# Optimization experiments

Measured on AMD Instinct MI355X. Metric: run time of the kernel, lower is better.

Reference implementation:

```python
import jax, jax.numpy as jnp
import numpy as np

K = 5        # spline kernel_size per dim (dim=2 -> 25 kernel weights)
NPG = 75     # MNIST superpixel nodes per graph


def _spline_conv(x, src, dst, pseudo, emask, W, root, bias):
    """SplineConv, dim=2, kernel_size=5, degree=1 open splines, aggr='mean'.
    emask in {0,1} masks out coalesced-away (duplicate/self-loop) edges."""
    n = x.shape[0]
    v = jnp.clip(pseudo, 0.0, 1.0) * (K - 1)
    bot = jnp.clip(jnp.floor(v), 0, K - 2)
    frac = v - bot                                   # [E,2]
    bot = bot.astype(jnp.int32)
    xj = x[src] * emask[:, None]                     # [E,Fin] gathered source feats
    # aggregate-then-transform: acc[k,i,:] = sum over edges into i with basis k
    acc = jnp.zeros((K * K, n, x.shape[1]), x.dtype)
    for o0 in (0, 1):
        for o1 in (0, 1):
            w = (frac[:, 0] if o0 else 1.0 - frac[:, 0]) * (frac[:, 1] if o1 else 1.0 - frac[:, 1])
            kk = (bot[:, 0] + o0) + K * (bot[:, 1] + o1)
            acc = acc.at[kk, dst].add(w[:, None] * xj)
    out = jnp.einsum('knf,kfo->no', acc, W)
    deg = jax.ops.segment_sum(emask, dst, num_segments=n)
    return out / jnp.maximum(deg, 1.0)[:, None] + x @ root + bias


def _pool(x, pos, valid, batch, src, dst, emask, size, G, B):
    """voxel_grid + max_pool with static shapes: S=B*G*G clusters, masked."""
    S = B * G * G
    c = jnp.clip(jnp.floor(pos / size).astype(jnp.int32), 0, G - 1)
    cl = batch * (G * G) + c[:, 1] * G + c[:, 0]
    xm = jnp.where(valid[:, None] > 0, x, -1e30)
    px = jax.ops.segment_max(xm, cl, num_segments=S)
    cnt = jax.ops.segment_sum(valid, cl, num_segments=S)
    sval = (cnt > 0).astype(x.dtype)
    px = jnp.where(sval[:, None] > 0, px, 0.0)
    ppos = jax.ops.segment_sum(pos * valid[:, None], cl, num_segments=S) / jnp.maximum(cnt, 1.0)[:, None]
    nb = jnp.arange(S, dtype=jnp.int32) // (G * G)
    # remap edges to clusters; mask self loops and duplicates (= coalesce)
    nsrc, ndst = cl[src], cl[dst]
    m = (emask > 0) & (nsrc != ndst)
    a0 = jnp.where(m, nsrc, S)
    b0 = jnp.where(m, ndst, S)
    order = jnp.lexsort((b0, a0))
    a, b = a0[order], b0[order]
    first = jnp.concatenate([jnp.array([True]), (a[1:] != a[:-1]) | (b[1:] != b[:-1])])
    keep = jnp.zeros(src.shape[0], dtype=bool).at[order].set(first & (a < S))
    kf = keep.astype(x.dtype)
    # T.Cartesian(cat=False, norm=True): pseudo = (pos_src-pos_dst)/(2*max|.|)+0.5
    cart = ppos[nsrc] - ppos[ndst]
    amax = jnp.maximum(jnp.max(jnp.abs(cart) * kf[:, None]), 1e-12)
    pseudo = cart / (2.0 * amax) + 0.5
    return px, ppos, sval, nb, nsrc, ndst, kf, pseudo


def _forward(x, pos, src, dst, W1, r1, b1, W2, r2, b2, W3, r3, b3, fw1, fb1, fw2, fb2):
    N = x.shape[0]
    B = N // NPG
    batch = jnp.arange(N, dtype=jnp.int32) // NPG
    valid = jnp.ones((N,), x.dtype)
    emask = jnp.ones((src.shape[0],), x.dtype)
    cart = pos[src] - pos[dst]
    pseudo = cart / (2.0 * jnp.maximum(jnp.max(jnp.abs(cart)), 1e-12)) + 0.5
    x = jax.nn.elu(_spline_conv(x, src, dst, pseudo, emask, W1, r1, b1))
    x, pos, valid, batch, src, dst, emask, pseudo = _pool(x, pos, valid, batch, src, dst, emask, 5.0, 6, B)
    x = jax.nn.elu(_spline_conv(x, src, dst, pseudo, emask, W2, r2, b2))
    x, pos, valid, batch, src, dst, emask, pseudo = _pool(x, pos, valid, batch, src, dst, emask, 7.0, 5, B)
    x = jax.nn.elu(_spline_conv(x, src, dst, pseudo, emask, W3, r3, b3))
    # max_pool_x(cluster, x, batch, size=4): 2x2 voxel grid (size=14, end=27.99)
    c = jnp.clip(jnp.floor(pos / 14.0).astype(jnp.int32), 0, 1)
    cl = batch * 4 + c[:, 1] * 2 + c[:, 0]
    xm = jnp.where(valid[:, None] > 0, x, -1e30)
    px = jax.ops.segment_max(xm, cl, num_segments=B * 4)
    cnt = jax.ops.segment_sum(valid, cl, num_segments=B * 4)
    px = jnp.where((cnt > 0)[:, None], px, 0.0)
    h = jax.nn.elu(px.reshape(B, 4 * 64) @ fw1.T + fb1)
    logits = h @ fw2.T + fb2  # F.dropout is identity in eval mode
    return jax.nn.log_softmax(logits, axis=1)


def setup_inputs() -> dict:
    key = jax.random.key(0)
    ks = jax.random.split(key, 16)
    B, EPG = 1024, 1392
    N = B * NPG
    x = jax.random.normal(ks[0], (N, 1), jnp.float32)
    pos = jax.random.uniform(ks[1], (N, 2), jnp.float32) * 27.99
    s = jax.random.randint(ks[2], (B, EPG), 0, NPG)
    d = (s + 1 + jax.random.randint(ks[3], (B, EPG), 0, NPG - 1)) % NPG  # no self loops
    off = (jnp.arange(B, dtype=jnp.int32) * NPG)[:, None]
    src = (s + off).reshape(-1)
    dst = (d + off).reshape(-1)
    rn = lambda k, sh, sc: jax.random.normal(k, sh, jnp.float32) * sc
    return dict(x=x, pos=pos, src=src, dst=dst,
                W1=rn(ks[4], (25, 1, 32), 0.2), r1=rn(ks[5], (1, 32), 0.2), b1=jnp.zeros((32,), jnp.float32),
                W2=rn(ks[6], (25, 32, 64), 0.05), r2=rn(ks[7], (32, 64), 0.1), b2=jnp.zeros((64,), jnp.float32),
                W3=rn(ks[8], (25, 64, 64), 0.04), r3=rn(ks[9], (64, 64), 0.08), b3=jnp.zeros((64,), jnp.float32),
                fw1=rn(ks[10], (128, 256), 0.06), fb1=jnp.zeros((128,), jnp.float32),
                fw2=rn(ks[11], (10, 128), 0.09), fb2=jnp.zeros((10,), jnp.float32))


def reference(x, pos, src, dst, W1, r1, b1, W2, r2, b2, W3, r3, b3, fw1, fb1, fw2, fb2):
    return _forward(x, pos, src, dst, W1, r1, b1, W2, r2, b2, W3, r3, b3, fw1, fb1, fw2, fb2)
```

## Files before the change

kernel.cpp:

```cpp
#include <hip/hip_runtime.h>
#include <math.h>

#define NPG 75
#define KDIM 5

typedef _Float16 half8 __attribute__((ext_vector_type(8)));
typedef _Float16 half4 __attribute__((ext_vector_type(4)));
typedef float f32x4 __attribute__((ext_vector_type(4)));

__device__ __forceinline__ float eluf(float v){ return v > 0.f ? v : expf(v) - 1.f; }

__device__ __forceinline__ unsigned fenc(float f){
    unsigned u = __float_as_uint(f);
    return (u & 0x80000000u) ? ~u : (u | 0x80000000u);
}
__device__ __forceinline__ float fdec(unsigned u){
    return (u & 0x80000000u) ? __uint_as_float(u & 0x7FFFFFFFu) : __uint_as_float(~u);
}

__device__ __forceinline__ void fma25(float (&r)[25], const float (&wx)[5], const float (&wyx)[5]){
    #pragma unroll
    for (int b1 = 0; b1 < 5; b1++)
        #pragma unroll
        for (int b0 = 0; b0 < 5; b0++)
            asm("v_fmac_f32 %0, %1, %2" : "+v"(r[b1 * 5 + b0]) : "v"(wx[b0]), "v"(wyx[b1]));
}

__device__ __forceinline__ void spline2(float c0, float c1, float am, int* kks, float* wsp){
    float denom = 2.f * fmaxf(am, 1e-12f);
    float p0 = c0 / denom + 0.5f;
    float p1 = c1 / denom + 0.5f;
    p0 = fminf(fmaxf(p0, 0.f), 1.f) * 4.f;
    p1 = fminf(fmaxf(p1, 0.f), 1.f) * 4.f;
    float b0 = fminf(floorf(p0), 3.f);
    float b1 = fminf(floorf(p1), 3.f);
    float f0 = p0 - b0, f1 = p1 - b1;
    int i0 = (int)b0, i1 = (int)b1;
    wsp[0] = (1.f - f0) * (1.f - f1); kks[0] = i0     + KDIM *  i1;
    wsp[1] =        f0  * (1.f - f1); kks[1] = i0 + 1 + KDIM *  i1;
    wsp[2] = (1.f - f0) *        f1 ; kks[2] = i0     + KDIM * (i1 + 1);
    wsp[3] =        f0  *        f1 ; kks[3] = i0 + 1 + KDIM * (i1 + 1);
}

__global__ __launch_bounds__(256) void amax0_k(
        const float* __restrict__ pos, const int* __restrict__ src,
        const int* __restrict__ dst, int E4, unsigned* __restrict__ outbits){
    float cand = 0.f;
    for (int i = blockIdx.x * 256 + threadIdx.x; i < E4; i += gridDim.x * 256){
        int4 s4 = ((const int4*)src)[i];
        int4 d4 = ((const int4*)dst)[i];
        #pragma unroll
        for (int k = 0; k < 4; k++){
            int s = (&s4.x)[k], d = (&d4.x)[k];
            float c0 = pos[s*2]   - pos[d*2];
            float c1 = pos[s*2+1] - pos[d*2+1];
            cand = fmaxf(cand, fmaxf(fabsf(c0), fabsf(c1)));
        }
    }
    __shared__ float sm[256];
    sm[threadIdx.x] = cand; __syncthreads();
    for (int o = 128; o > 0; o >>= 1){
        if (threadIdx.x < o) sm[threadIdx.x] = fmaxf(sm[threadIdx.x], sm[threadIdx.x + o]);
        __syncthreads();
    }
    if (threadIdx.x == 0) atomicMax(outbits, __float_as_uint(sm[0]));
}

__global__ __launch_bounds__(512) void conv1pool1_k(
        const float* __restrict__ x, const float* __restrict__ pos,
        const int* __restrict__ src, const int* __restrict__ dst, int EPG,
        const unsigned* __restrict__ amaxp,
        const float* __restrict__ W1, const float* __restrict__ r1, const float* __restrict__ b1,
        float* __restrict__ px1, float* __restrict__ pp1, float* __restrict__ sv1,
        int* __restrict__ cl1){
    __shared__ __align__(16) float acc[NPG * 28];
    __shared__ float deg[NPG];
    __shared__ float xl[NPG], p0l[NPG], p1l[NPG];
    __shared__ int   cli[NPG];
    __shared__ float W1s[800], r1s[32], b1s[32];
    __shared__ unsigned px[36 * 32];
    __shared__ float cnt[36], ps[72];

    const int b = blockIdx.x, t = threadIdx.x;
    const int n0 = b * NPG, e0 = b * EPG;

    for (int i = t; i < NPG * 28; i += 512) acc[i] = 0.f;
    for (int i = t; i < 36 * 32; i += 512) px[i] = 0u;
    if (t < NPG) deg[t] = 0.f;
    if (t < 36) cnt[t] = 0.f;
    if (t < 72) ps[t] = 0.f;
    for (int i = t; i < 800; i += 512) W1s[i] = W1[i];
    if (t < 32){ r1s[t] = r1[t]; b1s[t] = b1[t]; }
    if (t < NPG){
        float p0 = pos[(n0 + t) * 2], p1 = pos[(n0 + t) * 2 + 1];
        xl[t] = x[n0 + t]; p0l[t] = p0; p1l[t] = p1;
        int c0 = min(max((int)floorf(p0 / 5.f), 0), 5);
        int c1 = min(max((int)floorf(p1 / 5.f), 0), 5);
        int c = c1 * 6 + c0;
        cli[t] = c;
        cl1[n0 + t] = b * 36 + c;
    }
    __syncthreads();

    const int o = t & 31;
    float wreg[25];
    #pragma unroll
    for (int k = 0; k < 25; k++) wreg[k] = W1s[k * 32 + o];
    const float rro = r1s[o], bbo = b1s[o];

    if (t < NPG){
        int c = cli[t];
        atomicAdd(&cnt[c], 1.f);
        atomicAdd(&ps[c*2],     p0l[t]);
        atomicAdd(&ps[c*2 + 1], p1l[t]);
    }

    const float am = __uint_as_float(*amaxp);
    for (int e = t; e < EPG; e += 512){
        int s = src[e0 + e] - n0;
        int d = dst[e0 + e] - n0;
        float c0 = p0l[s] - p0l[d];
        float c1 = p1l[s] - p1l[d];
        int kks[4]; float wsp[4];
        spline2(c0, c1, am, kks, wsp);
        float xv = xl[s];
        #pragma unroll
        for (int c = 0; c < 4; c++) atomicAdd(&acc[d*28 + kks[c]], wsp[c] * xv);
        atomicAdd(&deg[d], 1.f);
    }
    __syncthreads();

    const int ii = t >> 5;
    #pragma unroll
    for (int r = 0; r < 5; r++){
        int i = ii + r * 16;
        if (i < NPG){
            const float4* ar = (const float4*)(acc + i * 28);
            float s = 0.f;
            #pragma unroll
            for (int q = 0; q < 7; q++){
                float4 aq = ar[q];
                s += aq.x * wreg[q*4];
                if (q*4 + 1 < 25) s += aq.y * wreg[q*4 + 1];
                if (q*4 + 2 < 25) s += aq.z * wreg[q*4 + 2];
                if (q*4 + 3 < 25) s += aq.w * wreg[q*4 + 3];
            }
            float v = s / fmaxf(deg[i], 1.f) + xl[i] * rro + bbo;
            v = eluf(v);
            atomicMax(&px[cli[i]*32 + o], fenc(v));
        }
    }
    __syncthreads();

    for (int idx = t; idx < 36 * 32; idx += 512){
        int s_ = idx >> 5;
        px1[(size_t)(b*36)*32 + idx] = (cnt[s_] > 0.f) ? fdec(px[idx]) : 0.f;
    }
    if (t < 36){
        float c = cnt[t], m = fmaxf(c, 1.f);
        pp1[(b*36 + t)*2]     = ps[t*2] / m;
        pp1[(b*36 + t)*2 + 1] = ps[t*2 + 1] / m;
        sv1[b*36 + t] = (c > 0.f) ? 1.f : 0.f;
    }
}

template<int GG, int NN>
__global__ __launch_bounds__(1024) void dedup_csr_k(
        const int* src_in, const int* dst_in,
        const int* __restrict__ clmap, const unsigned char* __restrict__ kf_in,
        unsigned char* kf_out, int* es_out, int* ed_out,
        const float* __restrict__ pp, int EPG,
        int* __restrict__ easrc, float2* __restrict__ ecart,
        int* __restrict__ rowptr2, int* __restrict__ kcnt, unsigned* __restrict__ amaxbits){
    __shared__ unsigned pm[GG * GG];
    __shared__ float degs[GG];
    __shared__ int rs[GG + 1];
    __shared__ int cur[GG];
    __shared__ float red[16];
    __shared__ int   clS[NN];
    __shared__ float ppS[2 * GG];

    const int b = blockIdx.x, t = threadIdx.x;
    const int lane = t & 63, wid = t >> 6;
    const int e0 = b * EPG;
    const int cbase = b * GG;

    for (int i = t; i < GG * GG; i += 1024) pm[i] = 0xFFFFFFFFu;
    if (t < GG) degs[t] = 0.f;
    if (t < NN) clS[t] = clmap[b * NN + t] - cbase;
    if (t < 2 * GG) ppS[t] = pp[cbase * 2 + t];
    __syncthreads();

    const int niter = (EPG + 1023) / 1024;
    int la[2], lb[2]; bool lm[2];
    const int nbase = b * NN;
    for (int it = 0; it < niter; it++){
        int e = t + it * 1024;
        lm[it] = false;
        if (e < EPG){
            int a  = clS[src_in[e0 + e] - nbase];
            int bb = clS[dst_in[e0 + e] - nbase];
            la[it] = a; lb[it] = bb;
            es_out[e0 + e] = cbase + a; ed_out[e0 + e] = cbase + bb;
            bool m = (kf_in ? (kf_in[e0 + e] != 0) : true) && (a != bb);
            lm[it] = m;
            if (m) atomicMin(&pm[a * GG + bb], (unsigned)e);
        }
    }
    __syncthreads();

    float cand = 0.f;
    bool kept[2]; float lc0[2], lc1[2];
    for (int it = 0; it < niter; it++){
        int e = t + it * 1024;
        kept[it] = false;
        if (e < EPG){
            bool k = false;
            if (lm[it]) k = (pm[la[it] * GG + lb[it]] == (unsigned)e);
            kept[it] = k;
            if (kf_out) kf_out[e0 + e] = k ? 1 : 0;
            if (k){
                atomicAdd(&degs[lb[it]], 1.f);
                float c0 = ppS[la[it]*2]     - ppS[lb[it]*2];
                float c1 = ppS[la[it]*2 + 1] - ppS[lb[it]*2 + 1];
                lc0[it] = c0; lc1[it] = c1;
                cand = fmaxf(cand, fmaxf(fabsf(c0), fabsf(c1)));
            }
        }
    }
    #pragma unroll
    for (int o = 1; o < 64; o <<= 1) cand = fmaxf(cand, __shfl_xor(cand, o, 64));
    if (lane == 0) red[wid] = cand;
    __syncthreads();
    if (t == 0){
        float m = red[0];
        #pragma unroll
        for (int i = 1; i < 16; i++) m = fmaxf(m, red[i]);
        atomicMax(amaxbits, __float_as_uint(m));
    }
    if (t < 64){
        int v = (t < GG) ? (int)degs[t] : 0;
        int incl = v;
        #pragma unroll
        for (int o = 1; o < 64; o <<= 1){
            int u = __shfl_up(incl, o, 64);
            if (t >= o) incl += u;
        }
        if (t == 0) rs[0] = 0;
        if (t < GG) rs[t + 1] = incl;
    }
    __syncthreads();
    if (t < GG){
        rowptr2[(cbase + t)*2]     = e0 + rs[t];
        rowptr2[(cbase + t)*2 + 1] = e0 + rs[t + 1];
        cur[t] = rs[t];
    }
    if (t == 0) kcnt[b] = rs[GG];
    __syncthreads();
    for (int it = 0; it < niter; it++){
        if (kept[it]){
            int slot = atomicAdd(&cur[lb[it]], 1);
            easrc[e0 + slot] = cbase + la[it];
            ecart[e0 + slot] = make_float2(lc0[it], lc1[it]);
        }
    }
}

__global__ void espline_k(const float2* __restrict__ ecart, const unsigned* __restrict__ amaxp,
                          const int* __restrict__ kcnt, int EPG, int E,
                          float* __restrict__ edata){
    int i = blockIdx.x * 256 + threadIdx.x;
    if (i >= E) return;
    int b = i / EPG;
    if (i - b * EPG >= kcnt[b]) return;
    float2 c = ecart[i];
    float am = __uint_as_float(*amaxp);
    float denom = 2.f * fmaxf(am, 1e-12f);
    float p0 = fminf(fmaxf(c.x / denom + 0.5f, 0.f), 1.f) * 4.f;
    float p1 = fminf(fmaxf(c.y / denom + 0.5f, 0.f), 1.f) * 4.f;
    float b0 = fminf(floorf(p0), 3.f);
    float b1 = fminf(floorf(p1), 3.f);
    int i0 = (int)b0, i1 = (int)b1;
    float f0 = p0 - b0, f1 = p1 - b1;
    float wx[5], wy[5];
    #pragma unroll
    for (int k = 0; k < 5; k++){
        wx[k] = (k == i0) ? (1.f - f0) : ((k == i0 + 1) ? f0 : 0.f);
        wy[k] = (k == i1) ? (1.f - f1) : ((k == i1 + 1) ? f1 : 0.f);
    }
    float* d = edata + (size_t)i * 8;
    *(float4*)(d)     = make_float4(wx[0], wx[1], wx[2], wx[3]);
    *(float4*)(d + 4) = make_float4(wy[0], wy[1], wy[2], wy[3]);
}

template<int CIN, int G>
__global__ __launch_bounds__(256) void pool_mid_k(
        const float* __restrict__ xin, const float* __restrict__ ppin,
        const float* __restrict__ svin, float size,
        float* __restrict__ pxout, float* __restrict__ ppout, float* __restrict__ svout,
        int* __restrict__ clout){
    __shared__ unsigned px[G * G * 64];
    __shared__ float cnt[G * G], ps[2 * G * G];
    __shared__ int cli[CIN];
    const int b = blockIdx.x, t = threadIdx.x;

    for (int i = t; i < G * G * 64; i += 256) px[i] = 0u;
    if (t < G * G){ cnt[t] = 0.f; ps[t*2] = 0.f; ps[t*2 + 1] = 0.f; }
    if (t < CIN){
        float v  = svin[b*CIN + t];
        float p0 = ppin[(b*CIN + t)*2], p1 = ppin[(b*CIN + t)*2 + 1];
        int c0 = min(max((int)floorf(p0 / size), 0), G - 1);
        int c1 = min(max((int)floorf(p1 / size), 0), G - 1);
        int c = c1 * G + c0;
        cli[t] = (v > 0.f) ? c : -1;
        clout[b*CIN + t] = b * G * G + c;
    }
    __syncthreads();
    if (t < CIN && cli[t] >= 0){
        int c = cli[t];
        atomicAdd(&cnt[c], 1.f);
        atomicAdd(&ps[c*2],     ppin[(b*CIN + t)*2]);
        atomicAdd(&ps[c*2 + 1], ppin[(b*CIN + t)*2 + 1]);
    }
    __syncthreads();
    for (int idx = t; idx < CIN * 64; idx += 256){
        int i = idx >> 6, f = idx & 63;
        if (cli[i] >= 0)
            atomicMax(&px[cli[i]*64 + f], fenc(xin[(size_t)(b*CIN + i)*64 + f]));
    }
    __syncthreads();
    for (int idx = t; idx < G * G * 64; idx += 256){
        int s_ = idx >> 6;
        pxout[(size_t)(b*G*G)*64 + idx] = (cnt[s_] > 0.f) ? fdec(px[idx]) : 0.f;
    }
    if (t < G * G){
        float c = cnt[t], m = fmaxf(c, 1.f);
        ppout[(b*G*G + t)*2]     = ps[t*2] / m;
        ppout[(b*G*G + t)*2 + 1] = ps[t*2 + 1] / m;
        svout[b*G*G + t] = (c > 0.f) ? 1.f : 0.f;
    }
}

__global__ void wswz_k(const float* __restrict__ W, const float* __restrict__ root,
                       int FIN, _Float16* __restrict__ Wz){
    int gid = blockIdx.x * 256 + threadIdx.x;
    int KT = 26 * FIN;
    if (gid >= KT * 64) return;
    int k = gid >> 6, n = gid & 63;
    float v = (k < 25 * FIN) ? W[(size_t)k * 64 + n] : root[(size_t)(k - 25 * FIN) * 64 + n];
    int kt = k >> 5, kr = k & 31, quad = kr >> 3, j = kr & 7;
    int lane = (quad << 4) | (n & 15);
    int nt = n >> 4;
    Wz[(((size_t)(kt * 4 + nt) * 64 + lane) << 3) + j] = (_Float16)v;
}

template<int FIN>
__global__ __launch_bounds__(64) void conv_gather_k(
        const float* __restrict__ x, const int* __restrict__ easrc,
        const float* __restrict__ edata,
        const int* __restrict__ rowptr2, int n, _Float16* __restrict__ Aout){
    constexpr int KTOT = 26 * FIN;
    const int lane = threadIdx.x;
    const int node = blockIdx.x;
    const int row0 = rowptr2[node*2], row1 = rowptr2[node*2 + 1];
    constexpr int STEP = (FIN == 32) ? 2 : 1;
    const int sub = (FIN == 32) ? (lane >> 5) : 0;
    const int f = lane & (FIN - 1);

    float r[25];
    #pragma unroll
    for (int b = 0; b < 25; b++) r[b] = 0.f;

    int iCur = row0 + sub;
    int aNext = 0;
    float4 waC, wbC;
    float xvCur = 0.f;
    if (iCur < row1){
        int aCur = easrc[iCur];
        const float* d = edata + (size_t)iCur * 8;
        waC = *(const float4*)(d); wbC = *(const float4*)(d + 4);
        xvCur = x[(size_t)aCur * FIN + f];
        int i1 = (iCur + STEP < row1) ? iCur + STEP : iCur;
        aNext = easrc[i1];
    }
    for (; iCur < row1; iCur += STEP){
        int iN  = iCur + STEP;
        int iNs = (iN < row1) ? iN : iCur;
        int iN2 = (iN + STEP < row1) ? iN + STEP : iNs;
        const float* dn = edata + (size_t)iNs * 8;
        float4 waN = *(const float4*)(dn);
        float4 wbN = *(const float4*)(dn + 4);
        float xvN = x[(size_t)aNext * FIN + f];
        int aN2 = easrc[iN2];
        float wx4 = 1.f - (waC.x + waC.y + waC.z + waC.w);
        float wy4 = 1.f - (wbC.x + wbC.y + wbC.z + wbC.w);
        float wx[5]  = {waC.x, waC.y, waC.z, waC.w, wx4};
        float wyx[5] = {wbC.x * xvCur, wbC.y * xvCur, wbC.z * xvCur, wbC.w * xvCur, wy4 * xvCur};
        fma25(r, wx, wyx);
        waC = waN; wbC = wbN; xvCur = xvN; aNext = aN2;
    }

    if (FIN == 32){
        #pragma unroll
        for (int b = 0; b < 25; b++) r[b] += __shfl_xor(r[b], 32, 64);
    }

    float inv = 1.f / (float)max(row1 - row0, 1);
    _Float16* dstrow = Aout + (size_t)node * KTOT;
    if (FIN == 64){
        #pragma unroll
        for (int b = 0; b < 25; b++) dstrow[b * 64 + f] = (_Float16)(r[b] * inv);
        dstrow[25 * 64 + f] = (_Float16)x[(size_t)node * 64 + f];
    } else {
        #pragma unroll
        for (int b = 0; b < 25; b++)
            if ((b & 1) == sub) dstrow[b * 32 + f] = (_Float16)(r[b] * inv);
        if (sub == 0) dstrow[25 * 32 + f] = (_Float16)x[(size_t)node * 32 + f];
    }
}

template<int KTOT, int SPLITK>
__global__ __launch_bounds__(256) void conv_mfma_k(
        const _Float16* __restrict__ A, const _Float16* __restrict__ Wz,
        int M, float* __restrict__ Cpart){
    constexpr int NSTEP = KTOT / SPLITK / 32;
    const int w = threadIdx.x >> 6, lane = threadIdx.x & 63;
    const int m0 = blockIdx.x * 64 + w * 16;
    const int kt0 = blockIdx.y * NSTEP;
    const int quad = lane >> 4;

    f32x4 acc[4];
    #pragma unroll
    for (int nt = 0; nt < 4; nt++) acc[nt] = (f32x4){0.f, 0.f, 0.f, 0.f};

    const half8* __restrict__ Arow = (const half8*)(A + (size_t)(m0 + (lane & 15)) * KTOT);
    const half8* __restrict__ Wp   = (const half8*)Wz + (size_t)kt0 * 4 * 64 + lane;

    for (int kt = 0; kt < NSTEP; kt++){
        half8 a = Arow[(kt0 + kt) * 4 + quad];
        #pragma unroll
        for (int nt = 0; nt < 4; nt++){
            half8 b = Wp[(kt * 4 + nt) * 64];
            acc[nt] = __builtin_amdgcn_mfma_f32_16x16x32_f16(a, b, acc[nt], 0, 0, 0);
        }
    }

    float* cp = Cpart + ((size_t)blockIdx.y * M + m0) * 64;
    const int r = quad * 4, c = lane & 15;
    #pragma unroll
    for (int nt = 0; nt < 4; nt++)
        #pragma unroll
        for (int i = 0; i < 4; i++)
            cp[(size_t)(r + i) * 64 + nt * 16 + c] = acc[nt][i];
}

template<int SPLITK>
__global__ void conv_epi_k(const float* __restrict__ Cpart, const float* __restrict__ bias,
                           int M, float* __restrict__ out){
    int gid = blockIdx.x * 256 + threadIdx.x;
    if (gid >= M * 64) return;
    int c = gid & 63;
    float v = bias[c];
    #pragma unroll
    for (int s = 0; s < SPLITK; s++) v += Cpart[(size_t)s * M * 64 + gid];
    out[gid] = eluf(v);
}

__global__ __launch_bounds__(256) void final_k(
        const float* __restrict__ xin, const float* __restrict__ ppin,
        const float* __restrict__ svin,
        const float* __restrict__ fw1, const float* __restrict__ fb1,
        const float* __restrict__ fw2, const float* __restrict__ fb2,
        float* __restrict__ out){
    __shared__ unsigned px[4 * 64];
    __shared__ float cnt[4];
    __shared__ int cli[25];
    __shared__ float xr[256];
    __shared__ float h[128];
    __shared__ float lg[10];
    __shared__ float lse;
    const int b = blockIdx.x, t = threadIdx.x;

    if (t < 4*64) px[t] = 0u;
    if (t < 4) cnt[t] = 0.f;
    if (t < 25){
        float v  = svin[b*25 + t];
        float p0 = ppin[(b*25 + t)*2], p1 = ppin[(b*25 + t)*2 + 1];
        int c0 = min(max((int)floorf(p0 / 14.f), 0), 1);
        int c1 = min(max((int)floorf(p1 / 14.f), 0), 1);
        int c = c1 * 2 + c0;
        cli[t] = (v > 0.f) ? c : -1;
    }
    __syncthreads();
    if (t < 25 && cli[t] >= 0) atomicAdd(&cnt[cli[t]], 1.f);
    __syncthreads();
    for (int idx = t; idx < 25 * 64; idx += 256){
        int i = idx >> 6, f = idx & 63;
        if (cli[i] >= 0)
            atomicMax(&px[cli[i]*64 + f], fenc(xin[(size_t)(b*25 + i)*64 + f]));
    }
    __syncthreads();
    xr[t] = (cnt[t >> 6] > 0.f) ? fdec(px[t]) : 0.f;
    __syncthreads();
    if (t < 128){
        float s = fb1[t];
        const float* wrow = fw1 + (size_t)t * 256;
        #pragma unroll 8
        for (int i = 0; i < 256; i++) s += xr[i] * wrow[i];
        h[t] = eluf(s);
    }
    __syncthreads();
    if (t < 10){
        float s2 = fb2[t];
        const float* w2 = fw2 + (size_t)t * 128;
        for (int j = 0; j < 128; j++) s2 += h[j] * w2[j];
        lg[t] = s2;
    }
    __syncthreads();
    if (t == 0){
        float m = lg[0];
        for (int c = 1; c < 10; c++) m = fmaxf(m, lg[c]);
        float se = 0.f;
        for (int c = 0; c < 10; c++) se += expf(lg[c] - m);
        lse = m + logf(se);
    }
    __syncthreads();
    if (t < 10) out[(size_t)b*10 + t] = lg[t] - lse;
}

extern "C" void kernel_launch(void* const* d_in, const int* in_sizes, int n_in,
                              void* d_out, int out_size, void* d_ws, size_t ws_size,
                              hipStream_t stream) {
    const float* x   = (const float*)d_in[0];
    const float* pos = (const float*)d_in[1];
    const int*   src = (const int*)d_in[2];
    const int*   dst = (const int*)d_in[3];
    const float* W1  = (const float*)d_in[4];
    const float* r1  = (const float*)d_in[5];
    const float* b1  = (const float*)d_in[6];
    const float* W2  = (const float*)d_in[7];
    const float* r2  = (const float*)d_in[8];
    const float* b2  = (const float*)d_in[9];
    const float* W3  = (const float*)d_in[10];
    const float* r3  = (const float*)d_in[11];
    const float* b3  = (const float*)d_in[12];
    const float* fw1 = (const float*)d_in[13];
    const float* fb1 = (const float*)d_in[14];
    const float* fw2 = (const float*)d_in[15];
    const float* fb2 = (const float*)d_in[16];
    float* out = (float*)d_out;

    const int N   = in_sizes[0];
    const int E   = in_sizes[2];
    const int B   = N / NPG;
    const int EPG = E / B;
    const int S1  = B * 36;
    const int S2  = B * 25;

    float* w = (float*)d_ws;
    size_t off = 0;
    auto alloc = [&](size_t nelem){ size_t o = off; off += (nelem + 63) & ~(size_t)63; return o; };

    size_t o_scal = alloc(4);
    size_t o_px1  = alloc((size_t)S1 * 32);
    size_t o_pp1  = alloc((size_t)S1 * 2);
    size_t o_sv1  = alloc(S1);
    size_t o_cl1  = alloc(N);
    size_t o_kf1  = alloc((E + 3) / 4);
    size_t o_es1  = alloc(E);
    size_t o_ed1  = alloc(E);
    size_t o_easrc= alloc(E);
    size_t o_ecart= alloc((size_t)2 * E);
    size_t o_edat = alloc((size_t)8 * E);
    size_t o_kcnt = alloc(B);
    size_t o_rp2  = alloc((size_t)2 * S1);
    size_t o_rp3  = alloc((size_t)2 * S2);
    size_t o_out2 = alloc((size_t)S1 * 64);
    size_t o_cl2  = alloc(S1);
    size_t o_px2  = alloc((size_t)S2 * 64);
    size_t o_pp2  = alloc((size_t)S2 * 2);
    size_t o_sv2  = alloc(S2);
    size_t o_out3 = alloc((size_t)S2 * 64);
    size_t o_wz   = alloc((size_t)26 * 64 * 64 / 2 + 64);
    size_t cpElems = (size_t)2 * S1 * 64 > (size_t)4 * S2 * 64 ? (size_t)2 * S1 * 64 : (size_t)4 * S2 * 64;
    size_t o_cp   = alloc(cpElems);
    size_t accAhalfs = (size_t)S1 * 832 > (size_t)S2 * 1664 ? (size_t)S1 * 832 : (size_t)S2 * 1664;
    size_t o_accA = alloc((accAhalfs + 1) / 2);

    hipMemsetAsync(w + o_scal, 0, 4 * sizeof(float), stream);

    unsigned* scal = (unsigned*)(w + o_scal);
    _Float16* Wz   = (_Float16*)(w + o_wz);
    _Float16* A16  = (_Float16*)(w + o_accA);
    auto nb = [](long long t){ return (unsigned)((t + 255) / 256); };

    const int E4 = E / 4;
    int gA = (E4 + 255) / 256; if (gA > 512) gA = 512;
    amax0_k<<<gA, 256, 0, stream>>>(pos, src, dst, E4, scal + 0);
    conv1pool1_k<<<B, 512, 0, stream>>>(x, pos, src, dst, EPG, scal + 0, W1, r1, b1,
                                        w + o_px1, w + o_pp1, w + o_sv1, (int*)(w + o_cl1));

    dedup_csr_k<36, NPG><<<B, 1024, 0, stream>>>(
        src, dst, (int*)(w + o_cl1), nullptr,
        (unsigned char*)(w + o_kf1), (int*)(w + o_es1), (int*)(w + o_ed1),
        w + o_pp1, EPG, (int*)(w + o_easrc), (float2*)(w + o_ecart),
        (int*)(w + o_rp2), (int*)(w + o_kcnt), scal + 1);
    espline_k<<<nb(E), 256, 0, stream>>>((float2*)(w + o_ecart), scal + 1,
                                         (int*)(w + o_kcnt), EPG, E, w + o_edat);

    wswz_k<<<nb(26 * 32 * 64), 256, 0, stream>>>(W2, r2, 32, Wz);
    conv_gather_k<32><<<S1, 64, 0, stream>>>(
        w + o_px1, (int*)(w + o_easrc), w + o_edat,
        (int*)(w + o_rp2), S1, A16);
    {
        dim3 g(S1 / 64, 2);
        conv_mfma_k<832, 2><<<g, 256, 0, stream>>>(A16, Wz, S1, w + o_cp);
    }
    conv_epi_k<2><<<nb((long long)S1 * 64), 256, 0, stream>>>(w + o_cp, b2, S1, w + o_out2);

    pool_mid_k<36, 5><<<B, 256, 0, stream>>>(
        w + o_out2, w + o_pp1, w + o_sv1, 7.f,
        w + o_px2, w + o_pp2, w + o_sv2, (int*)(w + o_cl2));

    dedup_csr_k<25, 36><<<B, 1024, 0, stream>>>(
        (int*)(w + o_es1), (int*)(w + o_ed1), (int*)(w + o_cl2), (unsigned char*)(w + o_kf1),
        nullptr, (int*)(w + o_es1), (int*)(w + o_ed1),
        w + o_pp2, EPG, (int*)(w + o_easrc), (float2*)(w + o_ecart),
        (int*)(w + o_rp3), (int*)(w + o_kcnt), scal + 2);
    espline_k<<<nb(E), 256, 0, stream>>>((float2*)(w + o_ecart), scal + 2,
                                         (int*)(w + o_kcnt), EPG, E, w + o_edat);

    wswz_k<<<nb(26 * 64 * 64), 256, 0, stream>>>(W3, r3, 64, Wz);
    conv_gather_k<64><<<S2, 64, 0, stream>>>(
        w + o_px2, (int*)(w + o_easrc), w + o_edat,
        (int*)(w + o_rp3), S2, A16);
    {
        dim3 g(S2 / 64, 4);
        conv_mfma_k<1664, 4><<<g, 256, 0, stream>>>(A16, Wz, S2, w + o_cp);
    }
    conv_epi_k<4><<<nb((long long)S2 * 64), 256, 0, stream>>>(w + o_cp, b3, S2, w + o_out3);

    final_k<<<B, 256, 0, stream>>>(w + o_out3, w + o_pp2, w + o_sv2,
                                   fw1, fb1, fw2, fb2, out);
}
```

Before: 375.0 us.

## Fuse pipeline stages to cut kernel launches and drop split-K partials

Removes the espline kernels by computing the spline basis inline in the gather from the raw edge offsets, and merges pool2 with the second dedup/CSR pass into one kernel. Drops split-K in the MFMA conv so bias and ELU are applied in its epilogue, replaces the two weight-swizzle launches with one, and vectorizes the fc1 loop. The aim is fewer launches and less intermediate global traffic. In exchange the MFMA grids are smaller, with no K parallelism, and the gather does extra per-edge arithmetic.

After: 380.4 us. About the same (+1.4%).

```diff
diff --git a/kernel.cpp b/kernel.cpp
--- a/kernel.cpp
+++ b/kernel.cpp
@@ -83,6 +83,8 @@
 
     const int b = blockIdx.x, t = threadIdx.x;
     const int n0 = b * NPG, e0 = b * EPG;
+
+    const float am = __uint_as_float(*amaxp);
 
     for (int i = t; i < NPG * 28; i += 512) acc[i] = 0.f;
     for (int i = t; i < 36 * 32; i += 512) px[i] = 0u;
@@ -115,7 +117,6 @@
         atomicAdd(&ps[c*2 + 1], p1l[t]);
     }
 
-    const float am = __uint_as_float(*amaxp);
     for (int e = t; e < EPG; e += 512){
         int s = src[e0 + e] - n0;
         int d = dst[e0 + e] - n0;
@@ -266,87 +267,155 @@
     }
 }
 
-__global__ void espline_k(const float2* __restrict__ ecart, const unsigned* __restrict__ amaxp,
-                          const int* __restrict__ kcnt, int EPG, int E,
-                          float* __restrict__ edata){
-    int i = blockIdx.x * 256 + threadIdx.x;
-    if (i >= E) return;
-    int b = i / EPG;
-    if (i - b * EPG >= kcnt[b]) return;
-    float2 c = ecart[i];
-    float am = __uint_as_float(*amaxp);
-    float denom = 2.f * fmaxf(am, 1e-12f);
-    float p0 = fminf(fmaxf(c.x / denom + 0.5f, 0.f), 1.f) * 4.f;
-    float p1 = fminf(fmaxf(c.y / denom + 0.5f, 0.f), 1.f) * 4.f;
-    float b0 = fminf(floorf(p0), 3.f);
-    float b1 = fminf(floorf(p1), 3.f);
-    int i0 = (int)b0, i1 = (int)b1;
-    float f0 = p0 - b0, f1 = p1 - b1;
-    float wx[5], wy[5];
+__global__ __launch_bounds__(1024) void dedup_pool_k(
+        const int* __restrict__ src_in, const int* __restrict__ dst_in,
+        const unsigned char* __restrict__ kf_in,
+        const float* __restrict__ xin,
+        const float* __restrict__ pp1, const float* __restrict__ sv1,
+        int EPG,
+        float* __restrict__ px2, float* __restrict__ pp2, float* __restrict__ sv2,
+        int* __restrict__ easrc, float2* __restrict__ ecart,
+        int* __restrict__ rowptr2, int* __restrict__ kcnt, unsigned* __restrict__ amaxbits){
+    constexpr int GG = 25, NN = 36;
+    __shared__ unsigned pm[GG * GG];
+    __shared__ float degs[GG];
+    __shared__ int rs[GG + 1];
+    __shared__ int cur[GG];
+    __shared__ float red[16];
+    __shared__ int   clS[NN];
+    __shared__ int   vld[NN];
+    __shared__ float ppS[2 * GG];
+    __shared__ unsigned px[GG * 64];
+    __shared__ float cnt[GG], ps[2 * GG];
+
+    const int b = blockIdx.x, t = threadIdx.x;
+    const int lane = t & 63, wid = t >> 6;
+    const int e0 = b * EPG;
+    const int cbase = b * GG;
+    const int nb36  = b * NN;
+
+    for (int i = t; i < GG * GG; i += 1024) pm[i] = 0xFFFFFFFFu;
+    for (int i = t; i < GG * 64; i += 1024) px[i] = 0u;
+    if (t < GG){ degs[t] = 0.f; cnt[t] = 0.f; }
+    if (t < 2 * GG) ps[t] = 0.f;
+    if (t < NN){
+        float v  = sv1[nb36 + t];
+        float p0 = pp1[(nb36 + t)*2], p1 = pp1[(nb36 + t)*2 + 1];
+        int c0 = min(max((int)floorf(p0 / 7.f), 0), 4);
+        int c1 = min(max((int)floorf(p1 / 7.f), 0), 4);
+        clS[t] = c1 * 5 + c0;
+        vld[t] = (v > 0.f) ? 1 : 0;
+    }
+    __syncthreads();
+
+    if (t < NN && vld[t]){
+        int c = clS[t];
+        atomicAdd(&cnt[c], 1.f);
+        atomicAdd(&ps[c*2],     pp1[(nb36 + t)*2]);
+        atomicAdd(&ps[c*2 + 1], pp1[(nb36 + t)*2 + 1]);
+    }
+    for (int idx = t; idx < NN * 64; idx += 1024){
+        int i = idx >> 6, f = idx & 63;
+        if (vld[i])
+            atomicMax(&px[clS[i]*64 + f], fenc(xin[(size_t)(nb36 + i)*64 + f]));
+    }
+    const int niter = (EPG + 1023) / 1024;
+    int la[2], lb[2]; bool lm[2];
+    for (int it = 0; it < niter; it++){
+        int e = t + it * 1024;
+        lm[it] = false;
+        if (e < EPG){
+            int a  = clS[src_in[e0 + e] - nb36];
+            int bb = clS[dst_in[e0 + e] - nb36];
+            la[it] = a; lb[it] = bb;
+            bool m = (kf_in[e0 + e] != 0) && (a != bb);
+            lm[it] = m;
+            if (m) atomicMin(&pm[a * GG + bb], (unsigned)e);
+        }
+    }
+    __syncthreads();
+
+    if (t < GG){
+        float c = cnt[t], m = fmaxf(c, 1.f);
+        float q0 = ps[t*2] / m, q1 = ps[t*2 + 1] / m;
+        ppS[t*2] = q0; ppS[t*2 + 1] = q1;
+        pp2[(cbase + t)*2]     = q0;
+        pp2[(cbase + t)*2 + 1] = q1;
+        sv2[cbase + t] = (c > 0.f) ? 1.f : 0.f;
+    }
+    for (int idx = t; idx < GG * 64; idx += 1024){
+        int s_ = idx >> 6;
+        px2[(size_t)cbase*64 + idx] = (cnt[s_] > 0.f) ? fdec(px[idx]) : 0.f;
+    }
+    __syncthreads();
+
+    float cand = 0.f;
+    bool kept[2]; float lc0[2], lc1[2];
+    for (int it = 0; it < niter; it++){
+        int e = t + it * 1024;
+        kept[it] = false;
+        if (e < EPG){
+            bool k = false;
+            if (lm[it]) k = (pm[la[it] * GG + lb[it]] == (unsigned)e);
+            kept[it] = k;
+            if (k){
+                atomicAdd(&degs[lb[it]], 1.f);
+                float c0 = ppS[la[it]*2]     - ppS[lb[it]*2];
+                float c1 = ppS[la[it]*2 + 1] - ppS[lb[it]*2 + 1];
+                lc0[it] = c0; lc1[it] = c1;
+                cand = fmaxf(cand, fmaxf(fabsf(c0), fabsf(c1)));
+            }
+        }
+    }
     #pragma unroll
-    for (int k = 0; k < 5; k++){
-        wx[k] = (k == i0) ? (1.f - f0) : ((k == i0 + 1) ? f0 : 0.f);
-        wy[k] = (k == i1) ? (1.f - f1) : ((k == i1 + 1) ? f1 : 0.f);
-    }
-    float* d = edata + (size_t)i * 8;
-    *(float4*)(d)     = make_float4(wx[0], wx[1], wx[2], wx[3]);
-    *(float4*)(d + 4) = make_float4(wy[0], wy[1], wy[2], wy[3]);
-}
-
-template<int CIN, int G>
-__global__ __launch_bounds__(256) void pool_mid_k(
-        const float* __restrict__ xin, const float* __restrict__ ppin,
-        const float* __restrict__ svin, float size,
-        float* __restrict__ pxout, float* __restrict__ ppout, float* __restrict__ svout,
-        int* __restrict__ clout){
-    __shared__ unsigned px[G * G * 64];
-    __shared__ float cnt[G * G], ps[2 * G * G];
-    __shared__ int cli[CIN];
-    const int b = blockIdx.x, t = threadIdx.x;
-
-    for (int i = t; i < G * G * 64; i += 256) px[i] = 0u;
-    if (t < G * G){ cnt[t] = 0.f; ps[t*2] = 0.f; ps[t*2 + 1] = 0.f; }
-    if (t < CIN){
-        float v  = svin[b*CIN + t];
-        float p0 = ppin[(b*CIN + t)*2], p1 = ppin[(b*CIN + t)*2 + 1];
-        int c0 = min(max((int)floorf(p0 / size), 0), G - 1);
-        int c1 = min(max((int)floorf(p1 / size), 0), G - 1);
-        int c = c1 * G + c0;
-        cli[t] = (v > 0.f) ? c : -1;
-        clout[b*CIN + t] = b * G * G + c;
-    }
-    __syncthreads();
-    if (t < CIN && cli[t] >= 0){
-        int c = cli[t];
-        atomicAdd(&cnt[c], 1.f);
-        atomicAdd(&ps[c*2],     ppin[(b*CIN + t)*2]);
-        atomicAdd(&ps[c*2 + 1], ppin[(b*CIN + t)*2 + 1]);
-    }
-    __syncthreads();
-    for (int idx = t; idx < CIN * 64; idx += 256){
-        int i = idx >> 6, f = idx & 63;
-        if (cli[i] >= 0)
-            atomicMax(&px[cli[i]*64 + f], fenc(xin[(size_t)(b*CIN + i)*64 + f]));
-    }
-    __syncthreads();
-    for (int idx = t; idx < G * G * 64; idx += 256){
-        int s_ = idx >> 6;
-        pxout[(size_t)(b*G*G)*64 + idx] = (cnt[s_] > 0.f) ? fdec(px[idx]) : 0.f;
-    }
-    if (t < G * G){
-        float c = cnt[t], m = fmaxf(c, 1.f);
-        ppout[(b*G*G + t)*2]     = ps[t*2] / m;
-        ppout[(b*G*G + t)*2 + 1] = ps[t*2 + 1] / m;
-        svout[b*G*G + t] = (c > 0.f) ? 1.f : 0.f;
-    }
-}
-
-__global__ void wswz_k(const float* __restrict__ W, const float* __restrict__ root,
-                       int FIN, _Float16* __restrict__ Wz){
+    for (int o = 1; o < 64; o <<= 1) cand = fmaxf(cand, __shfl_xor(cand, o, 64));
+    if (lane == 0) red[wid] = cand;
+    __syncthreads();
+    if (t == 0){
+        float m = red[0];
+        #pragma unroll
+        for (int i = 1; i < 16; i++) m = fmaxf(m, red[i]);
+        atomicMax(amaxbits, __float_as_uint(m));
+    }
+    if (t < 64){
+        int v = (t < GG) ? (int)degs[t] : 0;
+        int incl = v;
+        #pragma unroll
+        for (int o = 1; o < 64; o <<= 1){
+            int u = __shfl_up(incl, o, 64);
+            if (t >= o) incl += u;
+        }
+        if (t == 0) rs[0] = 0;
+        if (t < GG) rs[t + 1] = incl;
+    }
+    __syncthreads();
+    if (t < GG){
+        rowptr2[(cbase + t)*2]     = e0 + rs[t];
+        rowptr2[(cbase + t)*2 + 1] = e0 + rs[t + 1];
+        cur[t] = rs[t];
+    }
+    if (t == 0) kcnt[b] = rs[GG];
+    __syncthreads();
+    for (int it = 0; it < niter; it++){
+        if (kept[it]){
+            int slot = atomicAdd(&cur[lb[it]], 1);
+            easrc[e0 + slot] = cbase + la[it];
+            ecart[e0 + slot] = make_float2(lc0[it], lc1[it]);
+        }
+    }
+}
+
+__global__ void wswz2_k(const float* __restrict__ W2, const float* __restrict__ r2,
+                        const float* __restrict__ W3, const float* __restrict__ r3,
+                        _Float16* __restrict__ Wz2, _Float16* __restrict__ Wz3){
     int gid = blockIdx.x * 256 + threadIdx.x;
-    int KT = 26 * FIN;
-    if (gid >= KT * 64) return;
-    int k = gid >> 6, n = gid & 63;
+    const int T2 = 26 * 32 * 64;
+    const int T3 = 26 * 64 * 64;
+    const float* W; const float* root; _Float16* Wz; int FIN; int g;
+    if (gid < T2){ W = W2; root = r2; Wz = Wz2; FIN = 32; g = gid; }
+    else if (gid < T2 + T3){ W = W3; root = r3; Wz = Wz3; FIN = 64; g = gid - T2; }
+    else return;
+    int k = g >> 6, n = g & 63;
     float v = (k < 25 * FIN) ? W[(size_t)k * 64 + n] : root[(size_t)(k - 25 * FIN) * 64 + n];
     int kt = k >> 5, kr = k & 31, quad = kr >> 3, j = kr & 7;
     int lane = (quad << 4) | (n & 15);
@@ -357,8 +426,8 @@
 template<int FIN>
 __global__ __launch_bounds__(64) void conv_gather_k(
         const float* __restrict__ x, const int* __restrict__ easrc,
-        const float* __restrict__ edata,
-        const int* __restrict__ rowptr2, int n, _Float16* __restrict__ Aout){
+        const float2* __restrict__ ecart, const unsigned* __restrict__ amaxp,
+        const int* __restrict__ rowptr2, _Float16* __restrict__ Aout){
     constexpr int KTOT = 26 * FIN;
     const int lane = threadIdx.x;
     const int node = blockIdx.x;
@@ -367,18 +436,20 @@
     const int sub = (FIN == 32) ? (lane >> 5) : 0;
     const int f = lane & (FIN - 1);
 
+    const float am = __uint_as_float(*amaxp);
+    const float denom = 2.f * fmaxf(am, 1e-12f);
+
     float r[25];
     #pragma unroll
     for (int b = 0; b < 25; b++) r[b] = 0.f;
 
     int iCur = row0 + sub;
     int aNext = 0;
-    float4 waC, wbC;
+    float2 ccC = make_float2(0.f, 0.f);
     float xvCur = 0.f;
     if (iCur < row1){
         int aCur = easrc[iCur];
-        const float* d = edata + (size_t)iCur * 8;
-        waC = *(const float4*)(d); wbC = *(const float4*)(d + 4);
+        ccC = ecart[iCur];
         xvCur = x[(size_t)aCur * FIN + f];
         int i1 = (iCur + STEP < row1) ? iCur + STEP : iCur;
         aNext = easrc[i1];
@@ -387,17 +458,24 @@
         int iN  = iCur + STEP;
         int iNs = (iN < row1) ? iN : iCur;
         int iN2 = (iN + STEP < row1) ? iN + STEP : iNs;
-        const float* dn = edata + (size_t)iNs * 8;
-        float4 waN = *(const float4*)(dn);
-        float4 wbN = *(const float4*)(dn + 4);
+        float2 ccN = ecart[iNs];
         float xvN = x[(size_t)aNext * FIN + f];
         int aN2 = easrc[iN2];
-        float wx4 = 1.f - (waC.x + waC.y + waC.z + waC.w);
-        float wy4 = 1.f - (wbC.x + wbC.y + wbC.z + wbC.w);
-        float wx[5]  = {waC.x, waC.y, waC.z, waC.w, wx4};
-        float wyx[5] = {wbC.x * xvCur, wbC.y * xvCur, wbC.z * xvCur, wbC.w * xvCur, wy4 * xvCur};
+        float p0 = fminf(fmaxf(ccC.x / denom + 0.5f, 0.f), 1.f) * 4.f;
+        float p1 = fminf(fmaxf(ccC.y / denom + 0.5f, 0.f), 1.f) * 4.f;
+        float b0 = fminf(floorf(p0), 3.f);
+        float b1 = fminf(floorf(p1), 3.f);
+        int i0 = (int)b0, i1 = (int)b1;
+        float f0 = p0 - b0, f1 = p1 - b1;
+        float wx[5], wyx[5];
+        #pragma unroll
+        for (int k = 0; k < 5; k++){
+            wx[k] = (k == i0) ? (1.f - f0) : ((k == i0 + 1) ? f0 : 0.f);
+            float wy = (k == i1) ? (1.f - f1) : ((k == i1 + 1) ? f1 : 0.f);
+            wyx[k] = wy * xvCur;
+        }
         fma25(r, wx, wyx);
-        waC = waN; wbC = wbN; xvCur = xvN; aNext = aN2;
+        ccC = ccN; xvCur = xvN; aNext = aN2;
     }
 
     if (FIN == 32){
@@ -419,14 +497,13 @@
     }
 }
 
-template<int KTOT, int SPLITK>
+template<int KTOT>
 __global__ __launch_bounds__(256) void conv_mfma_k(
         const _Float16* __restrict__ A, const _Float16* __restrict__ Wz,
-        int M, float* __restrict__ Cpart){
-    constexpr int NSTEP = KTOT / SPLITK / 32;
+        const float* __restrict__ bias, int M, float* __restrict__ out){
+    constexpr int NSTEP = KTOT / 32;
     const int w = threadIdx.x >> 6, lane = threadIdx.x & 63;
     const int m0 = blockIdx.x * 64 + w * 16;
-    const int kt0 = blockIdx.y * NSTEP;
     const int quad = lane >> 4;
 
     f32x4 acc[4];
@@ -434,10 +511,10 @@
     for (int nt = 0; nt < 4; nt++) acc[nt] = (f32x4){0.f, 0.f, 0.f, 0.f};
 
     const half8* __restrict__ Arow = (const half8*)(A + (size_t)(m0 + (lane & 15)) * KTOT);
-    const half8* __restrict__ Wp   = (const half8*)Wz + (size_t)kt0 * 4 * 64 + lane;
+    const half8* __restrict__ Wp   = (const half8*)Wz + lane;
 
     for (int kt = 0; kt < NSTEP; kt++){
-        half8 a = Arow[(kt0 + kt) * 4 + quad];
+        half8 a = Arow[kt * 4 + quad];
         #pragma unroll
         for (int nt = 0; nt < 4; nt++){
             half8 b = Wp[(kt * 4 + nt) * 64];
@@ -445,25 +522,15 @@
         }
     }
 
-    float* cp = Cpart + ((size_t)blockIdx.y * M + m0) * 64;
+    float* cp = out + (size_t)m0 * 64;
     const int r = quad * 4, c = lane & 15;
     #pragma unroll
-    for (int nt = 0; nt < 4; nt++)
+    for (int nt = 0; nt < 4; nt++){
+        float bv = bias[nt * 16 + c];
         #pragma unroll
         for (int i = 0; i < 4; i++)
-            cp[(size_t)(r + i) * 64 + nt * 16 + c] = acc[nt][i];
-}
-
-template<int SPLITK>
-__global__ void conv_epi_k(const float* __restrict__ Cpart, const float* __restrict__ bias,
-                           int M, float* __restrict__ out){
-    int gid = blockIdx.x * 256 + threadIdx.x;
-    if (gid >= M * 64) return;
-    int c = gid & 63;
-    float v = bias[c];
-    #pragma unroll
-    for (int s = 0; s < SPLITK; s++) v += Cpart[(size_t)s * M * 64 + gid];
-    out[gid] = eluf(v);
+            cp[(size_t)(r + i) * 64 + nt * 16 + c] = eluf(acc[nt][i] + bv);
+    }
 }
 
 __global__ __launch_bounds__(256) void final_k(
@@ -504,9 +571,15 @@
     __syncthreads();
     if (t < 128){
         float s = fb1[t];
-        const float* wrow = fw1 + (size_t)t * 256;
-        #pragma unroll 8
-        for (int i = 0; i < 256; i++) s += xr[i] * wrow[i];
+        const float4* wrow = (const float4*)(fw1 + (size_t)t * 256);
+        #pragma unroll 4
+        for (int i = 0; i < 64; i++){
+            float4 q = wrow[i];
+            s += xr[i*4]   * q.x;
+            s += xr[i*4+1] * q.y;
+            s += xr[i*4+2] * q.z;
+            s += xr[i*4+3] * q.w;
+        }
         h[t] = eluf(s);
     }
     __syncthreads();
@@ -571,28 +644,28 @@
     size_t o_ed1  = alloc(E);
     size_t o_easrc= alloc(E);
     size_t o_ecart= alloc((size_t)2 * E);
-    size_t o_edat = alloc((size_t)8 * E);
     size_t o_kcnt = alloc(B);
     size_t o_rp2  = alloc((size_t)2 * S1);
     size_t o_rp3  = alloc((size_t)2 * S2);
     size_t o_out2 = alloc((size_t)S1 * 64);
-    size_t o_cl2  = alloc(S1);
     size_t o_px2  = alloc((size_t)S2 * 64);
     size_t o_pp2  = alloc((size_t)S2 * 2);
     size_t o_sv2  = alloc(S2);
     size_t o_out3 = alloc((size_t)S2 * 64);
-    size_t o_wz   = alloc((size_t)26 * 64 * 64 / 2 + 64);
-    size_t cpElems = (size_t)2 * S1 * 64 > (size_t)4 * S2 * 64 ? (size_t)2 * S1 * 64 : (size_t)4 * S2 * 64;
-    size_t o_cp   = alloc(cpElems);
+    size_t o_wz2  = alloc((size_t)26 * 32 * 64 / 2 + 64);
+    size_t o_wz3  = alloc((size_t)26 * 64 * 64 / 2 + 64);
     size_t accAhalfs = (size_t)S1 * 832 > (size_t)S2 * 1664 ? (size_t)S1 * 832 : (size_t)S2 * 1664;
     size_t o_accA = alloc((accAhalfs + 1) / 2);
 
     hipMemsetAsync(w + o_scal, 0, 4 * sizeof(float), stream);
 
     unsigned* scal = (unsigned*)(w + o_scal);
-    _Float16* Wz   = (_Float16*)(w + o_wz);
+    _Float16* Wz2  = (_Float16*)(w + o_wz2);
+    _Float16* Wz3  = (_Float16*)(w + o_wz3);
     _Float16* A16  = (_Float16*)(w + o_accA);
     auto nb = [](long long t){ return (unsigned)((t + 255) / 256); };
+
+    wswz2_k<<<nb(26 * 32 * 64 + 26 * 64 * 64), 256, 0, stream>>>(W2, r2, W3, r3, Wz2, Wz3);
 
     const int E4 = E / 4;
     int gA = (E4 + 255) / 256; if (gA > 512) gA = 512;
@@ -605,40 +678,23 @@
         (unsigned char*)(w + o_kf1), (int*)(w + o_es1), (int*)(w + o_ed1),
         w + o_pp1, EPG, (int*)(w + o_easrc), (float2*)(w + o_ecart),
         (int*)(w + o_rp2), (int*)(w + o_kcnt), scal + 1);
-    espline_k<<<nb(E), 256, 0, stream>>>((float2*)(w + o_ecart), scal + 1,
-                                         (int*)(w + o_kcnt), EPG, E, w + o_edat);
-
-    wswz_k<<<nb(26 * 32 * 64), 256, 0, stream>>>(W2, r2, 32, Wz);
+
     conv_gather_k<32><<<S1, 64, 0, stream>>>(
-        w + o_px1, (int*)(w + o_easrc), w + o_edat,
-        (int*)(w + o_rp2), S1, A16);
-    {
-        dim3 g(S1 / 64, 2);
-        conv_mfma_k<832, 2><<<g, 256, 0, stream>>>(A16, Wz, S1, w + o_cp);
-    }
-    conv_epi_k<2><<<nb((long long)S1 * 64), 256, 0, stream>>>(w + o_cp, b2, S1, w + o_out2);
-
-    pool_mid_k<36, 5><<<B, 256, 0, stream>>>(
-        w + o_out2, w + o_pp1, w + o_sv1, 7.f,
-        w + o_px2, w + o_pp2, w + o_sv2, (int*)(w + o_cl2));
-
-    dedup_csr_k<25, 36><<<B, 1024, 0, stream>>>(
-        (int*)(w + o_es1), (int*)(w + o_ed1), (int*)(w + o_cl2), (unsigned char*)(w + o_kf1),
-        nullptr, (int*)(w + o_es1), (int*)(w + o_ed1),
-        w + o_pp2, EPG, (int*)(w + o_easrc), (float2*)(w + o_ecart),
+        w + o_px1, (int*)(w + o_easrc), (const float2*)(w + o_ecart), scal + 1,
+        (int*)(w + o_rp2), A16);
+    conv_mfma_k<832><<<S1 / 64, 256, 0, stream>>>(A16, Wz2, b2, S1, w + o_out2);
+
+    dedup_pool_k<<<B, 1024, 0, stream>>>(
+        (int*)(w + o_es1), (int*)(w + o_ed1), (unsigned char*)(w + o_kf1),
+        w + o_out2, w + o_pp1, w + o_sv1, EPG,
+        w + o_px2, w + o_pp2, w + o_sv2,
+        (int*)(w + o_easrc), (float2*)(w + o_ecart),
         (int*)(w + o_rp3), (int*)(w + o_kcnt), scal + 2);
-    espline_k<<<nb(E), 256, 0, stream>>>((float2*)(w + o_ecart), scal + 2,
-                                         (int*)(w + o_kcnt), EPG, E, w + o_edat);
-
-    wswz_k<<<nb(26 * 64 * 64), 256, 0, stream>>>(W3, r3, 64, Wz);
+
     conv_gather_k<64><<<S2, 64, 0, stream>>>(
-        w + o_px2, (int*)(w + o_easrc), w + o_edat,
-        (int*)(w + o_rp3), S2, A16);
-    {
-        dim3 g(S2 / 64, 4);
-        conv_mfma_k<1664, 4><<<g, 256, 0, stream>>>(A16, Wz, S2, w + o_cp);
-    }
-    conv_epi_k<4><<<nb((long long)S2 * 64), 256, 0, stream>>>(w + o_cp, b3, S2, w + o_out3);
+        w + o_px2, (int*)(w + o_easrc), (const float2*)(w + o_ecart), scal + 2,
+        (int*)(w + o_rp3), A16);
+    conv_mfma_k<1664><<<S2 / 64, 256, 0, stream>>>(A16, Wz3, b3, S2, w + o_out3);
 
     final_k<<<B, 256, 0, stream>>>(w + o_out3, w + o_pp2, w + o_sv2,
                                    fw1, fb1, fw2, fb2, out);
```
